# Optimization experiments

Measured on AMD Instinct MI355X. Metric: run time of the kernel, lower is better.

## Reference

```python
import jax, jax.numpy as jnp
import numpy as np

HID = 1024
NH = 16
HD = HID // NH  # 64


def _lin_params(key, fan_in, fan_out):
    k1, k2 = jax.random.split(key)
    lim = 1.0 / np.sqrt(fan_in)
    W = jax.random.uniform(k1, (fan_in, fan_out), jnp.float32, -lim, lim)
    b = jax.random.uniform(k2, (fan_out,), jnp.float32, -lim, lim)
    return W, b


def setup_inputs() -> dict:
    key = jax.random.key(0)
    ks = jax.random.split(key, 12)
    B, S = 4, 1024
    inp = {
        'query': jax.random.normal(ks[0], (B, S, HID), jnp.float32),
        'key': jax.random.normal(ks[1], (B, S, HID), jnp.float32),
        'value': jax.random.normal(ks[2], (B, S, HID), jnp.float32),
    }
    inp['Wq'], inp['bq'] = _lin_params(ks[3], HID, HID)
    inp['Wk'], inp['bk'] = _lin_params(ks[4], HID, HID)
    inp['Wv'], inp['bv'] = _lin_params(ks[5], HID, HID)
    inp['Wp'], inp['bp'] = _lin_params(ks[6], HID, HID)
    inp['Wup'], inp['bup'] = _lin_params(ks[7], HD, 1)
    inp['Wud'], inp['bud'] = _lin_params(ks[8], HD, 1)
    inp['Wus'], inp['bus'] = _lin_params(ks[9], HID, NH)
    inp['Wo'], inp['bo'] = _lin_params(ks[10], HID, HID)
    return inp


def _split_heads(x, B, S):
    # [B,S,HID] -> [B,NH,S,HD]
    return x.reshape(B, S, NH, HD).transpose(0, 2, 1, 3)


def reference(query, key, value, Wq, bq, Wk, bk, Wv, bv, Wp, bp,
              Wup, bup, Wud, bud, Wus, bus, Wo, bo):
    B, S, _ = query.shape
    len_q = S

    q = query @ Wq + bq   # [B,S,HID]
    k = key @ Wk + bk
    v = value @ Wv + bv

    # Gaussian-window positional bias (per head, per query position)
    p = _split_heads(q @ Wp + bp, B, S)              # [B,NH,S,HD]
    tp = jnp.tanh(p)
    p_i = tp @ Wup + bup                             # [B,NH,S,1]
    z_i = tp @ Wud + bud                             # [B,NH,S,1]
    cen_pos = len_q * jax.nn.sigmoid(p_i)            # [B,NH,S,1]
    win_size = len_q * jax.nn.sigmoid(z_i)           # [B,NH,S,1]
    pos = jnp.arange(len_q, dtype=q.dtype)[None, None, None, :]  # [1,1,1,S]
    bias = (pos - cen_pos) ** 2 / (0.5 * win_size ** 2)          # [B,NH,S,S]

    # per-head alpha gate from raw query
    alpha = jax.nn.sigmoid(query @ Wus + bus)        # [B,S,NH]
    alpha = alpha.reshape(B, S, NH, 1).transpose(0, 2, 1, 3)  # [B,NH,S,1]

    qh = _split_heads(q, B, S)
    kh = _split_heads(k, B, S)
    vh = _split_heads(v, B, S)

    scale = 1.0 / jnp.sqrt(jnp.asarray(HD, q.dtype))
    scores = jnp.einsum('bhqd,bhkd->bhqk', qh, kh) * scale
    scores = scores - alpha * bias                   # inject gated Gaussian bias
    attn = jax.nn.softmax(scores, axis=-1)           # [B,NH,S,S]

    out = jnp.einsum('bhqk,bhkd->bhqd', attn, vh)    # [B,NH,S,HD]
    x = out.transpose(0, 2, 1, 3).reshape(B, S, HID)
    x = x @ Wo + bo
    return x, attn
```

## Files before the change

### kernel.cpp

```cpp
#include <hip/hip_runtime.h>
#include <hip/hip_bf16.h>
#include <math.h>

#define S_LEN 1024
#define HIDN  1024
#define NHEAD 16
#define HDIM  64
#define BATCH 4
#define MTOT  (BATCH * S_LEN)

typedef __attribute__((ext_vector_type(8))) short          bf16v8;
typedef __attribute__((ext_vector_type(8))) unsigned short u16v8;
typedef __attribute__((ext_vector_type(4))) unsigned short u16v4;
typedef __attribute__((ext_vector_type(4))) float          f32v4;

__device__ __forceinline__ unsigned short f2bf_rne(float x) {
    unsigned int u = __float_as_uint(x);
    unsigned int r = (u + 0x7fffu + ((u >> 16) & 1u)) >> 16;
    return (unsigned short)r;
}
__device__ __forceinline__ float bf2f(unsigned short h) {
    return __uint_as_float(((unsigned int)h) << 16);
}
__device__ __forceinline__ void split2(float x, unsigned short& h, unsigned short& l) {
    h = f2bf_rne(x);
    l = f2bf_rne(x - bf2f(h));
}

__global__ __launch_bounds__(256) void split_a(
    const float* __restrict__ X, unsigned short* __restrict__ H,
    unsigned short* __restrict__ L)
{
    const int i = blockIdx.x * 256 + threadIdx.x;
    const float4 x0 = ((const float4*)X)[2 * i];
    const float4 x1 = ((const float4*)X)[2 * i + 1];
    float xs[8] = {x0.x, x0.y, x0.z, x0.w, x1.x, x1.y, x1.z, x1.w};
    u16v8 h, l;
#pragma unroll
    for (int j = 0; j < 8; ++j) {
        unsigned short hh, ll;
        split2(xs[j], hh, ll);
        h[j] = hh; l[j] = ll;
    }
    ((u16v8*)H)[i] = h;
    ((u16v8*)L)[i] = l;
}

__global__ __launch_bounds__(256) void split_w(
    const float* __restrict__ W, unsigned short* __restrict__ H,
    unsigned short* __restrict__ L)
{
    __shared__ float T[64][65];
    const int t  = threadIdx.x;
    const int k0 = blockIdx.y * 64;
    const int n0 = blockIdx.x * 64;

    const int r = t >> 4;
    const int c = (t & 15) * 4;
#pragma unroll
    for (int i = 0; i < 4; ++i) {
        const int rr = r + i * 16;
        const float4 v = *(const float4*)&W[(size_t)(k0 + rr) * 1024 + n0 + c];
        T[rr][c + 0] = v.x; T[rr][c + 1] = v.y;
        T[rr][c + 2] = v.z; T[rr][c + 3] = v.w;
    }
    __syncthreads();

    const int n  = t >> 2;
    const int ko = (t & 3) * 16;
    u16v8 h0, h1, l0, l1;
#pragma unroll
    for (int kk = 0; kk < 8; ++kk) {
        unsigned short hh, ll;
        split2(T[ko + kk][n], hh, ll);
        h0[kk] = hh; l0[kk] = ll;
    }
#pragma unroll
    for (int kk = 0; kk < 8; ++kk) {
        unsigned short hh, ll;
        split2(T[ko + 8 + kk][n], hh, ll);
        h1[kk] = hh; l1[kk] = ll;
    }
    unsigned short* Hp = &H[(size_t)(n0 + n) * 1024 + k0 + ko];
    unsigned short* Lp = &L[(size_t)(n0 + n) * 1024 + k0 + ko];
    *(u16v8*)(Hp)     = h0;
    *(u16v8*)(Hp + 8) = h1;
    *(u16v8*)(Lp)     = l0;
    *(u16v8*)(Lp + 8) = l1;
}

__global__ __launch_bounds__(512, 2) void gemm_bf16x3(
    const unsigned short* __restrict__ Ah, const unsigned short* __restrict__ Al,
    const unsigned short* __restrict__ Bh, const unsigned short* __restrict__ Bl,
    const float* __restrict__ bias, float* __restrict__ Cf,
    unsigned short* __restrict__ Ch, unsigned short* __restrict__ Cl, int vt)
{
    __shared__ short Ash[128][40];
    __shared__ short Asl[128][40];
    __shared__ short Bsh[64][40];
    __shared__ short Bsl[64][40];

    const int t    = threadIdx.x;
    const int bm   = blockIdx.y * 128;
    const int bn   = blockIdx.x * 64;
    const int lane = t & 63;
    const int wid  = t >> 6;
    const int wr   = wid >> 1;
    const int wc   = wid & 1;
    const int fr   = lane & 15;
    const int fq   = lane >> 4;
    const int ks   = fq * 8;

    f32v4 zero = {0.f, 0.f, 0.f, 0.f};
    f32v4 acc[2][2];
#pragma unroll
    for (int i = 0; i < 2; ++i)
#pragma unroll
        for (int j = 0; j < 2; ++j) acc[i][j] = zero;

    const int sra = t >> 2;
    const int sca = (t & 3) * 8;
    const int tb  = t & 255;
    const int srb = tb >> 2;
    const int scb = (tb & 3) * 8;
    const bool isBl = (t >= 256);
    const unsigned short* pAh = &Ah[(size_t)(bm + sra) * 1024 + sca];
    const unsigned short* pAl = &Al[(size_t)(bm + sra) * 1024 + sca];
    const unsigned short* pB  = isBl ? &Bl[(size_t)(bn + srb) * 1024 + scb]
                                     : &Bh[(size_t)(bn + srb) * 1024 + scb];

    u16v8 rah, ral, rb;
    auto LOAD = [&](int k0) {
        rah = *(const u16v8*)(pAh + k0);
        ral = *(const u16v8*)(pAl + k0);
        rb  = *(const u16v8*)(pB  + k0);
    };

    LOAD(0);
    for (int k0 = 0; k0 < 1024; k0 += 32) {
        __syncthreads();
        *(u16v8*)&Ash[sra][sca] = rah;
        *(u16v8*)&Asl[sra][sca] = ral;
        if (isBl) *(u16v8*)&Bsl[srb][scb] = rb;
        else      *(u16v8*)&Bsh[srb][scb] = rb;
        __syncthreads();

        if (k0 + 32 < 1024) LOAD(k0 + 32);

        bf16v8 fah[2], fal[2], fbh[2], fbl[2];
#pragma unroll
        for (int i = 0; i < 2; ++i) {
            fah[i] = *(const bf16v8*)&Ash[wr * 32 + i * 16 + fr][ks];
            fal[i] = *(const bf16v8*)&Asl[wr * 32 + i * 16 + fr][ks];
        }
#pragma unroll
        for (int j = 0; j < 2; ++j) {
            fbh[j] = *(const bf16v8*)&Bsh[wc * 32 + j * 16 + fr][ks];
            fbl[j] = *(const bf16v8*)&Bsl[wc * 32 + j * 16 + fr][ks];
        }
#pragma unroll
        for (int i = 0; i < 2; ++i)
#pragma unroll
            for (int j = 0; j < 2; ++j) {
                acc[i][j] = __builtin_amdgcn_mfma_f32_16x16x32_bf16(
                    fah[i], fbh[j], acc[i][j], 0, 0, 0);
                acc[i][j] = __builtin_amdgcn_mfma_f32_16x16x32_bf16(
                    fah[i], fbl[j], acc[i][j], 0, 0, 0);
                acc[i][j] = __builtin_amdgcn_mfma_f32_16x16x32_bf16(
                    fal[i], fbh[j], acc[i][j], 0, 0, 0);
            }
    }

#pragma unroll
    for (int j = 0; j < 2; ++j) {
        const int col = bn + wc * 32 + j * 16 + fr;
        const float bb = bias[col];
#pragma unroll
        for (int i = 0; i < 2; ++i) {
            const int row0 = bm + wr * 32 + i * 16 + fq * 4;
            const f32v4 cv = acc[i][j];
            if (vt) {
                u16v4 h4, l4;
#pragma unroll
                for (int r = 0; r < 4; ++r) {
                    unsigned short hh, ll;
                    split2(cv[r] + bb, hh, ll);
                    h4[r] = hh; l4[r] = ll;
                }
                const size_t base =
                    ((size_t)((row0 >> 10) * 16 + (col >> 6)) * 64 + (col & 63)) * 1024
                    + (row0 & 1023);
                *(u16v4*)&Ch[base] = h4;
                *(u16v4*)&Cl[base] = l4;
            } else {
#pragma unroll
                for (int r = 0; r < 4; ++r) {
                    const float v = cv[r] + bb;
                    const size_t idx = (size_t)(row0 + r) * 1024 + col;
                    if (Cf) Cf[idx] = v;
                    if (Ch) {
                        unsigned short hh, ll;
                        split2(v, hh, ll);
                        Ch[idx] = hh; Cl[idx] = ll;
                    }
                }
            }
        }
    }
}

__global__ __launch_bounds__(256) void alpha_kernel(
    const float* __restrict__ X, const float* __restrict__ Wus,
    const float* __restrict__ bus, float* __restrict__ alpha)
{
    __shared__ float Ws[1024 * 16];
    const int t = threadIdx.x;
#pragma unroll
    for (int i = 0; i < 16; ++i) {
        const int idx = t + i * 256;
        *reinterpret_cast<float4*>(&Ws[idx * 4]) =
            *reinterpret_cast<const float4*>(&Wus[idx * 4]);
    }
    __syncthreads();

    const int r = t >> 4, c = t & 15;
    const size_t row = (size_t)blockIdx.x * 16 + r;
    const float* x = &X[row * 1024];
    float acc = 0.f;
    for (int kk = 0; kk < 1024; kk += 4) {
        const float4 xv = *reinterpret_cast<const float4*>(&x[kk]);
        acc = fmaf(xv.x, Ws[(kk + 0) * 16 + c], acc);
        acc = fmaf(xv.y, Ws[(kk + 1) * 16 + c], acc);
        acc = fmaf(xv.z, Ws[(kk + 2) * 16 + c], acc);
        acc = fmaf(xv.w, Ws[(kk + 3) * 16 + c], acc);
    }
    acc += bus[c];
    alpha[row * 16 + c] = 1.f / (1.f + expf(-acc));
}

__global__ __launch_bounds__(256) void posparam_kernel(
    const float* __restrict__ p, const float* __restrict__ alpha,
    const float* __restrict__ Wup, const float* __restrict__ bup,
    const float* __restrict__ Wud, const float* __restrict__ bud,
    float* __restrict__ cen, float* __restrict__ c0)
{
    __shared__ float wu[64], wd[64];
    const int t = threadIdx.x;
    if (t < 64) { wu[t] = Wup[t]; wd[t] = Wud[t]; }
    __syncthreads();

    const int tid = blockIdx.x * 256 + t;
    const int b = tid >> 14;
    const int h = (tid >> 10) & 15;
    const int s = tid & 1023;

    const float* pr = &p[((size_t)(b * 1024 + s)) * 1024 + h * 64];
    float ap = 0.f, az = 0.f;
#pragma unroll
    for (int d = 0; d < 64; d += 4) {
        const float4 pv = *reinterpret_cast<const float4*>(&pr[d]);
        const float t0 = tanhf(pv.x), t1 = tanhf(pv.y);
        const float t2 = tanhf(pv.z), t3 = tanhf(pv.w);
        ap += t0 * wu[d] + t1 * wu[d + 1] + t2 * wu[d + 2] + t3 * wu[d + 3];
        az += t0 * wd[d] + t1 * wd[d + 1] + t2 * wd[d + 2] + t3 * wd[d + 3];
    }
    ap += bup[0];
    az += bud[0];
    const float cenv = 1024.f / (1.f + expf(-ap));
    const float win  = 1024.f / (1.f + expf(-az));
    const float al   = alpha[(size_t)(b * 1024 + s) * 16 + h];
    const int oi = (b * 16 + h) * 1024 + s;
    cen[oi] = cenv;
    c0[oi]  = al * 2.f / (win * win);
}

#define M0_SHIFT 8.0f
__global__ __launch_bounds__(512, 2) void attn_fused(
    const unsigned short* __restrict__ qh, const unsigned short* __restrict__ ql,
    const unsigned short* __restrict__ kh, const unsigned short* __restrict__ kl,
    const unsigned short* __restrict__ vTh, const unsigned short* __restrict__ vTl,
    const float* __restrict__ cen, const float* __restrict__ c0,
    float* __restrict__ attn,
    unsigned short* __restrict__ oh, unsigned short* __restrict__ ol)
{
    __shared__ unsigned short KH[64][64], KL[64][64];
    __shared__ unsigned short VH[64][64], VL[64][64];
    __shared__ unsigned short PH[128][64], PL[128][64];
    __shared__ float CEN[128], C0S[128];
    __shared__ float LSUM[2][128];
    __shared__ float RINV[128];

    const int bid   = blockIdx.x;
    const int z     = ((bid >> 6) << 3) | (bid & 7);
    const int itile = (bid >> 3) & 7;
    const int i0    = itile * 128;
    const int bq    = z >> 4;
    const int hd    = z & 15;

    const int t    = threadIdx.x;
    const int lane = t & 63;
    const int wid  = t >> 6;
    const int wrp  = wid >> 1;
    const int wc   = wid & 1;
    const int fr   = lane & 15, fq = lane >> 4;

    if (t < 128) {
        CEN[t] = cen[(size_t)z * 1024 + i0 + t];
        C0S[t] = c0[(size_t)z * 1024 + i0 + t];
    }

    bf16v8 qfh_[2][2], qfl_[2][2];
#pragma unroll
    for (int i = 0; i < 2; ++i)
#pragma unroll
        for (int kk = 0; kk < 2; ++kk) {
            const size_t qa = (size_t)(bq * 1024 + i0 + wrp * 32 + i * 16 + fr) * 1024
                              + hd * 64 + kk * 32 + fq * 8;
            qfh_[i][kk] = *(const bf16v8*)&qh[qa];
            qfl_[i][kk] = *(const bf16v8*)&ql[qa];
        }

    float lsum[2][4];
#pragma unroll
    for (int i = 0; i < 2; ++i)
#pragma unroll
        for (int r = 0; r < 4; ++r) lsum[i][r] = 0.f;

    const f32v4 zero = {0.f, 0.f, 0.f, 0.f};

    const int srow = t >> 3;
    const int sseg = t & 7;
    const int ssl  = (sseg ^ (srow & 7)) * 8;
    const unsigned short* vhb = vTh + (size_t)z * 64 * 1024;
    const unsigned short* vlb = vTl + (size_t)z * 64 * 1024;

    u16v8 rkh, rkl, rvh, rvl;
    auto LOADK = [&](int j0) {
        const size_t ga = (size_t)(bq * 1024 + j0 + srow) * 1024 + hd * 64 + sseg * 8;
        rkh = *(const u16v8*)&kh[ga];
        rkl = *(const u16v8*)&kl[ga];
    };
    auto LOADV = [&](int j0) {
        const size_t va = (size_t)srow * 1024 + j0 + sseg * 8;
        rvh = *(const u16v8*)&vhb[va];
        rvl = *(const u16v8*)&vlb[va];
    };

    LOADK(0);
    for (int jt = 0; jt < 16; ++jt) {
        const int j0 = jt * 64;
        __syncthreads();
        *(u16v8*)&KH[srow][ssl] = rkh;
        *(u16v8*)&KL[srow][ssl] = rkl;
        __syncthreads();
        if (jt < 15) LOADK(j0 + 64);

        f32v4 acc[2][2];
#pragma unroll
        for (int i = 0; i < 2; ++i)
#pragma unroll
            for (int j2 = 0; j2 < 2; ++j2) acc[i][j2] = zero;

#pragma unroll
        for (int kk = 0; kk < 2; ++kk) {
            bf16v8 fbh[2], fbl[2];
#pragma unroll
            for (int j2 = 0; j2 < 2; ++j2) {
                const int rb = wc * 32 + j2 * 16 + fr;
                const int sb = ((kk * 4 + fq) ^ (rb & 7)) * 8;
                fbh[j2] = *(const bf16v8*)&KH[rb][sb];
                fbl[j2] = *(const bf16v8*)&KL[rb][sb];
            }
#pragma unroll
            for (int i = 0; i < 2; ++i)
#pragma unroll
                for (int j2 = 0; j2 < 2; ++j2) {
                    acc[i][j2] = __builtin_amdgcn_mfma_f32_16x16x32_bf16(
                        qfh_[i][kk], fbh[j2], acc[i][j2], 0, 0, 0);
                    acc[i][j2] = __builtin_amdgcn_mfma_f32_16x16x32_bf16(
                        qfh_[i][kk], fbl[j2], acc[i][j2], 0, 0, 0);
                    acc[i][j2] = __builtin_amdgcn_mfma_f32_16x16x32_bf16(
                        qfl_[i][kk], fbh[j2], acc[i][j2], 0, 0, 0);
                }
        }

#pragma unroll
        for (int i = 0; i < 2; ++i)
#pragma unroll
            for (int r = 0; r < 4; ++r) {
                const int row = wrp * 32 + i * 16 + fq * 4 + r;
                const float cv = CEN[row], cc = C0S[row];
                float al = 0.f;
#pragma unroll
                for (int j2 = 0; j2 < 2; ++j2) {
                    const int col = wc * 32 + j2 * 16 + fr;
                    const float dd = (float)(j0 + col) - cv;
                    const float s  = acc[i][j2][r] * 0.125f - cc * dd * dd;
                    al += __expf(s - M0_SHIFT);
                }
                lsum[i][r] += al;
            }
    }

#pragma unroll
    for (int i = 0; i < 2; ++i)
#pragma unroll
        for (int r = 0; r < 4; ++r) {
            float v = lsum[i][r];
            v += __shfl_xor(v, 1);
            v += __shfl_xor(v, 2);
            v += __shfl_xor(v, 4);
            v += __shfl_xor(v, 8);
            if (fr == 0) LSUM[wc][wrp * 32 + i * 16 + fq * 4 + r] = v;
        }
    __syncthreads();
    if (t < 128) RINV[t] = 1.f / (LSUM[0][t] + LSUM[1][t]);

    f32v4 acco[2][2];
#pragma unroll
    for (int i = 0; i < 2; ++i)
#pragma unroll
        for (int j = 0; j < 2; ++j) acco[i][j] = zero;

    float* attnZ = attn + (size_t)z * 1024 * 1024;

    LOADK(0);
    LOADV(0);
    for (int jt = 0; jt < 16; ++jt) {
        const int j0 = jt * 64;
        __syncthreads();
        *(u16v8*)&KH[srow][ssl] = rkh;
        *(u16v8*)&KL[srow][ssl] = rkl;
        *(u16v8*)&VH[srow][ssl] = rvh;
        *(u16v8*)&VL[srow][ssl] = rvl;
        __syncthreads();
        if (jt < 15) { LOADK(j0 + 64); LOADV(j0 + 64); }

        f32v4 acc[2][2];
#pragma unroll
        for (int i = 0; i < 2; ++i)
#pragma unroll
            for (int j2 = 0; j2 < 2; ++j2) acc[i][j2] = zero;

#pragma unroll
        for (int kk = 0; kk < 2; ++kk) {
            bf16v8 fbh[2], fbl[2];
#pragma unroll
            for (int j2 = 0; j2 < 2; ++j2) {
                const int rb = wc * 32 + j2 * 16 + fr;
                const int sb = ((kk * 4 + fq) ^ (rb & 7)) * 8;
                fbh[j2] = *(const bf16v8*)&KH[rb][sb];
                fbl[j2] = *(const bf16v8*)&KL[rb][sb];
            }
#pragma unroll
            for (int i = 0; i < 2; ++i)
#pragma unroll
                for (int j2 = 0; j2 < 2; ++j2) {
                    acc[i][j2] = __builtin_amdgcn_mfma_f32_16x16x32_bf16(
                        qfh_[i][kk], fbh[j2], acc[i][j2], 0, 0, 0);
                    acc[i][j2] = __builtin_amdgcn_mfma_f32_16x16x32_bf16(
                        qfh_[i][kk], fbl[j2], acc[i][j2], 0, 0, 0);
                    acc[i][j2] = __builtin_amdgcn_mfma_f32_16x16x32_bf16(
                        qfl_[i][kk], fbh[j2], acc[i][j2], 0, 0, 0);
                }
        }

#pragma unroll
        for (int i = 0; i < 2; ++i)
#pragma unroll
            for (int r = 0; r < 4; ++r) {
                const int row = wrp * 32 + i * 16 + fq * 4 + r;
                const float cv = CEN[row], cc = C0S[row], ri = RINV[row];
#pragma unroll
                for (int j2 = 0; j2 < 2; ++j2) {
                    const int col = wc * 32 + j2 * 16 + fr;
                    const float dd = (float)(j0 + col) - cv;
                    const float s  = acc[i][j2][r] * 0.125f - cc * dd * dd;
                    const float p  = __expf(s - M0_SHIFT) * ri;
                    attnZ[(size_t)(i0 + row) * 1024 + j0 + col] = p;
                    unsigned short hv, lv;
                    split2(p, hv, lv);
                    const int slot = ((col >> 3) ^ (row & 7)) * 8 + (col & 7);
                    PH[row][slot] = hv;
                    PL[row][slot] = lv;
                }
            }
        __syncthreads();

#pragma unroll
        for (int kk = 0; kk < 2; ++kk) {
            bf16v8 pah[2], pal[2], fbh[2], fbl[2];
#pragma unroll
            for (int iq = 0; iq < 2; ++iq) {
                const int rp = wrp * 32 + iq * 16 + fr;
                const int sp = ((kk * 4 + fq) ^ (rp & 7)) * 8;
                pah[iq] = *(const bf16v8*)&PH[rp][sp];
                pal[iq] = *(const bf16v8*)&PL[rp][sp];
            }
#pragma unroll
            for (int jd = 0; jd < 2; ++jd) {
                const int rb = wc * 32 + jd * 16 + fr;
                const int sb = ((kk * 4 + fq) ^ (rb & 7)) * 8;
                fbh[jd] = *(const bf16v8*)&VH[rb][sb];
                fbl[jd] = *(const bf16v8*)&VL[rb][sb];
            }
#pragma unroll
            for (int iq = 0; iq < 2; ++iq)
#pragma unroll
                for (int jd = 0; jd < 2; ++jd) {
                    acco[iq][jd] = __builtin_amdgcn_mfma_f32_16x16x32_bf16(
                        pah[iq], fbh[jd], acco[iq][jd], 0, 0, 0);
                    acco[iq][jd] = __builtin_amdgcn_mfma_f32_16x16x32_bf16(
                        pah[iq], fbl[jd], acco[iq][jd], 0, 0, 0);
                    acco[iq][jd] = __builtin_amdgcn_mfma_f32_16x16x32_bf16(
                        pal[iq], fbh[jd], acco[iq][jd], 0, 0, 0);
                }
        }
    }

#pragma unroll
    for (int jd = 0; jd < 2; ++jd) {
        const int dcol = wc * 32 + jd * 16 + fr;
#pragma unroll
        for (int iq = 0; iq < 2; ++iq) {
            const int row0 = i0 + wrp * 32 + iq * 16 + fq * 4;
            const f32v4 cv = acco[iq][jd];
#pragma unroll
            for (int r = 0; r < 4; ++r) {
                unsigned short hv, lv;
                split2(cv[r], hv, lv);
                const size_t idx = (size_t)(bq * 1024 + row0 + r) * 1024 + hd * 64 + dcol;
                oh[idx] = hv;
                ol[idx] = lv;
            }
        }
    }
}

extern "C" void kernel_launch(void* const* d_in, const int* in_sizes, int n_in,
                              void* d_out, int out_size, void* d_ws, size_t ws_size,
                              hipStream_t stream)
{
    const float* query = (const float*)d_in[0];
    const float* key_  = (const float*)d_in[1];
    const float* value = (const float*)d_in[2];
    const float* Wq  = (const float*)d_in[3];
    const float* bq  = (const float*)d_in[4];
    const float* Wk  = (const float*)d_in[5];
    const float* bk  = (const float*)d_in[6];
    const float* Wv  = (const float*)d_in[7];
    const float* bv  = (const float*)d_in[8];
    const float* Wp  = (const float*)d_in[9];
    const float* bp  = (const float*)d_in[10];
    const float* Wup = (const float*)d_in[11];
    const float* bup = (const float*)d_in[12];
    const float* Wud = (const float*)d_in[13];
    const float* bud = (const float*)d_in[14];
    const float* Wus = (const float*)d_in[15];
    const float* bus = (const float*)d_in[16];
    const float* Wo  = (const float*)d_in[17];
    const float* bo  = (const float*)d_in[18];

    float* x_out = (float*)d_out;
    float* attn  = x_out + (size_t)MTOT * HIDN;

    char* wsb = (char*)d_ws;
    unsigned short* qh  = (unsigned short*)(wsb);
    unsigned short* ql  = (unsigned short*)(wsb + (8u  << 20));
    unsigned short* kh  = (unsigned short*)(wsb + (16u << 20));
    unsigned short* kl  = (unsigned short*)(wsb + (24u << 20));
    unsigned short* vTh = (unsigned short*)(wsb + (32u << 20));
    unsigned short* vTl = (unsigned short*)(wsb + (40u << 20));
    float* p_ws  = (float*)(wsb + (48u << 20));
    unsigned short* oh = (unsigned short*)(wsb + (48u << 20));
    unsigned short* ol = (unsigned short*)(wsb + (56u << 20));
    float* alpha_ws = (float*)(wsb + (64u << 20));
    float* cen_ws   = (float*)(wsb + (64u << 20) + (256u << 10));
    float* c0_ws    = (float*)(wsb + (64u << 20) + (512u << 10));
    unsigned short* ah = (unsigned short*)attn;
    unsigned short* al = ah + (size_t)MTOT * HIDN;
    unsigned short* wh = al + (size_t)MTOT * HIDN;
    unsigned short* wl = wh + (size_t)HIDN * HIDN;
    unsigned short* w2h = qh;
    unsigned short* w2l = ql;

    const dim3 blk(256);
    const dim3 blk512(512);
    const dim3 gsplit_a(MTOT * HIDN / 8 / 256);
    const dim3 gsplit_w(16, 16);
    const dim3 ggemm(HIDN / 64, MTOT / 128);

    split_w<<<gsplit_w, blk, 0, stream>>>(Wq, wh, wl);
    split_a<<<gsplit_a, blk, 0, stream>>>(query, ah, al);
    gemm_bf16x3<<<ggemm, blk512, 0, stream>>>(ah, al, wh, wl, bq, nullptr, qh, ql, 0);
    split_w<<<gsplit_w, blk, 0, stream>>>(Wk, wh, wl);
    split_a<<<gsplit_a, blk, 0, stream>>>(key_, ah, al);
    gemm_bf16x3<<<ggemm, blk512, 0, stream>>>(ah, al, wh, wl, bk, nullptr, kh, kl, 0);
    split_w<<<gsplit_w, blk, 0, stream>>>(Wv, wh, wl);
    split_a<<<gsplit_a, blk, 0, stream>>>(value, ah, al);
    gemm_bf16x3<<<ggemm, blk512, 0, stream>>>(ah, al, wh, wl, bv, nullptr, vTh, vTl, 1);
    split_w<<<gsplit_w, blk, 0, stream>>>(Wp, wh, wl);
    gemm_bf16x3<<<ggemm, blk512, 0, stream>>>(qh, ql, wh, wl, bp, p_ws, nullptr, nullptr, 0);
    alpha_kernel<<<dim3(MTOT / 16), blk, 0, stream>>>(query, Wus, bus, alpha_ws);
    posparam_kernel<<<dim3((BATCH * NHEAD * S_LEN) / 256), blk, 0, stream>>>(
        p_ws, alpha_ws, Wup, bup, Wud, bud, cen_ws, c0_ws);
    attn_fused<<<dim3(512), blk512, 0, stream>>>(
        qh, ql, kh, kl, vTh, vTl, cen_ws, c0_ws, attn, oh, ol);
    split_w<<<gsplit_w, blk, 0, stream>>>(Wo, w2h, w2l);
    gemm_bf16x3<<<ggemm, blk512, 0, stream>>>(oh, ol, w2h, w2l, bo, x_out,
                                              nullptr, nullptr, 0);
}
```

Before: 390.4 us.

## Fuse activation splitting into GEMM loads and posparam into projection epilogue

The fp32 activations for the Q/K/V projections are now split into bf16 hi/lo pairs inside the GEMM's global load stage, which removes the separate split_a kernels and their round-trip of the split arrays through memory. The four weight splits are batched into one launch over a z-grid. The Wp projection epilogue now applies tanh, the Wup/Wud dot products, sigmoid and the alpha gating directly, so the fp32 p tensor is never written out and the posparam kernel is dropped. The cost is extra conversion ALU work in each GEMM's load path, repeated for every column tile that reads the same activation rows, plus an extra shared-memory reduction and barrier in the fused epilogue.

```diff
diff --git a/kernel.cpp b/kernel.cpp
--- a/kernel.cpp
+++ b/kernel.cpp
@@ -27,33 +27,19 @@
     l = f2bf_rne(x - bf2f(h));
 }
 
-__global__ __launch_bounds__(256) void split_a(
-    const float* __restrict__ X, unsigned short* __restrict__ H,
-    unsigned short* __restrict__ L)
-{
-    const int i = blockIdx.x * 256 + threadIdx.x;
-    const float4 x0 = ((const float4*)X)[2 * i];
-    const float4 x1 = ((const float4*)X)[2 * i + 1];
-    float xs[8] = {x0.x, x0.y, x0.z, x0.w, x1.x, x1.y, x1.z, x1.w};
-    u16v8 h, l;
-#pragma unroll
-    for (int j = 0; j < 8; ++j) {
-        unsigned short hh, ll;
-        split2(xs[j], hh, ll);
-        h[j] = hh; l[j] = ll;
-    }
-    ((u16v8*)H)[i] = h;
-    ((u16v8*)L)[i] = l;
-}
-
-__global__ __launch_bounds__(256) void split_w(
-    const float* __restrict__ W, unsigned short* __restrict__ H,
-    unsigned short* __restrict__ L)
+__global__ __launch_bounds__(256) void split_w4(
+    const float* __restrict__ W0, const float* __restrict__ W1,
+    const float* __restrict__ W2, const float* __restrict__ W3,
+    unsigned short* __restrict__ Hbase, unsigned short* __restrict__ Lbase)
 {
     __shared__ float T[64][65];
     const int t  = threadIdx.x;
     const int k0 = blockIdx.y * 64;
     const int n0 = blockIdx.x * 64;
+    const int z  = blockIdx.z;
+    const float* W = (z == 0) ? W0 : (z == 1) ? W1 : (z == 2) ? W2 : W3;
+    unsigned short* H = Hbase + (size_t)z * 1024 * 1024;
+    unsigned short* L = Lbase + (size_t)z * 1024 * 1024;
 
     const int r = t >> 4;
     const int c = (t & 15) * 4;
@@ -89,16 +75,23 @@
     *(u16v8*)(Lp + 8) = l1;
 }
 
-__global__ __launch_bounds__(512, 2) void gemm_bf16x3(
+template<int AF32, int EPI>
+__global__ __launch_bounds__(512, 2) void gemm_t(
+    const float* __restrict__ Af,
     const unsigned short* __restrict__ Ah, const unsigned short* __restrict__ Al,
     const unsigned short* __restrict__ Bh, const unsigned short* __restrict__ Bl,
     const float* __restrict__ bias, float* __restrict__ Cf,
-    unsigned short* __restrict__ Ch, unsigned short* __restrict__ Cl, int vt)
+    unsigned short* __restrict__ Ch, unsigned short* __restrict__ Cl,
+    const float* __restrict__ Wup, const float* __restrict__ Wud,
+    const float* __restrict__ bup, const float* __restrict__ bud,
+    const float* __restrict__ alpha, float* __restrict__ cenp,
+    float* __restrict__ c0p)
 {
     __shared__ short Ash[128][40];
     __shared__ short Asl[128][40];
     __shared__ short Bsh[64][40];
     __shared__ short Bsl[64][40];
+    __shared__ float PSUP[2][128], PSUD[2][128];
 
     const int t    = threadIdx.x;
     const int bm   = blockIdx.y * 128;
@@ -124,16 +117,29 @@
     const int srb = tb >> 2;
     const int scb = (tb & 3) * 8;
     const bool isBl = (t >= 256);
-    const unsigned short* pAh = &Ah[(size_t)(bm + sra) * 1024 + sca];
-    const unsigned short* pAl = &Al[(size_t)(bm + sra) * 1024 + sca];
-    const unsigned short* pB  = isBl ? &Bl[(size_t)(bn + srb) * 1024 + scb]
-                                     : &Bh[(size_t)(bn + srb) * 1024 + scb];
+    const unsigned short* pB = isBl ? &Bl[(size_t)(bn + srb) * 1024 + scb]
+                                    : &Bh[(size_t)(bn + srb) * 1024 + scb];
+    const float* pAf = AF32 ? &Af[(size_t)(bm + sra) * 1024 + sca] : nullptr;
+    const unsigned short* pAh = AF32 ? nullptr : &Ah[(size_t)(bm + sra) * 1024 + sca];
+    const unsigned short* pAl = AF32 ? nullptr : &Al[(size_t)(bm + sra) * 1024 + sca];
 
     u16v8 rah, ral, rb;
     auto LOAD = [&](int k0) {
-        rah = *(const u16v8*)(pAh + k0);
-        ral = *(const u16v8*)(pAl + k0);
-        rb  = *(const u16v8*)(pB  + k0);
+        if (AF32) {
+            const float4 a0 = *(const float4*)(pAf + k0);
+            const float4 a1 = *(const float4*)(pAf + k0 + 4);
+            const float xs[8] = {a0.x, a0.y, a0.z, a0.w, a1.x, a1.y, a1.z, a1.w};
+#pragma unroll
+            for (int e = 0; e < 8; ++e) {
+                unsigned short hh, ll;
+                split2(xs[e], hh, ll);
+                rah[e] = hh; ral[e] = ll;
+            }
+        } else {
+            rah = *(const u16v8*)(pAh + k0);
+            ral = *(const u16v8*)(pAl + k0);
+        }
+        rb = *(const u16v8*)(pB + k0);
     };
 
     LOAD(0);
@@ -171,6 +177,63 @@
             }
     }
 
+    if (EPI == 3) {
+        float wupj[2], wudj[2];
+        float bb[2];
+#pragma unroll
+        for (int j = 0; j < 2; ++j) {
+            const int colL = wc * 32 + j * 16 + fr;
+            wupj[j] = Wup[colL];
+            wudj[j] = Wud[colL];
+            bb[j]   = bias[bn + colL];
+        }
+        float su[2][4], sd[2][4];
+#pragma unroll
+        for (int i = 0; i < 2; ++i)
+#pragma unroll
+            for (int r = 0; r < 4; ++r) { su[i][r] = 0.f; sd[i][r] = 0.f; }
+#pragma unroll
+        for (int j = 0; j < 2; ++j)
+#pragma unroll
+            for (int i = 0; i < 2; ++i)
+#pragma unroll
+                for (int r = 0; r < 4; ++r) {
+                    const float tv = tanhf(acc[i][j][r] + bb[j]);
+                    su[i][r] = fmaf(tv, wupj[j], su[i][r]);
+                    sd[i][r] = fmaf(tv, wudj[j], sd[i][r]);
+                }
+#pragma unroll
+        for (int i = 0; i < 2; ++i)
+#pragma unroll
+            for (int r = 0; r < 4; ++r) {
+                float a = su[i][r], d = sd[i][r];
+                a += __shfl_xor(a, 1); d += __shfl_xor(d, 1);
+                a += __shfl_xor(a, 2); d += __shfl_xor(d, 2);
+                a += __shfl_xor(a, 4); d += __shfl_xor(d, 4);
+                a += __shfl_xor(a, 8); d += __shfl_xor(d, 8);
+                if (fr == 0) {
+                    const int row = wr * 32 + i * 16 + fq * 4 + r;
+                    PSUP[wc][row] = a;
+                    PSUD[wc][row] = d;
+                }
+            }
+        __syncthreads();
+        if (t < 128) {
+            const float ap = PSUP[0][t] + PSUP[1][t] + bup[0];
+            const float az = PSUD[0][t] + PSUD[1][t] + bud[0];
+            const float cenv = 1024.f / (1.f + expf(-ap));
+            const float win  = 1024.f / (1.f + expf(-az));
+            const int grow = bm + t;
+            const int hd   = bn >> 6;
+            const int zz   = (grow >> 10) * 16 + hd;
+            const int s    = grow & 1023;
+            const float al = alpha[(size_t)grow * 16 + hd];
+            cenp[(size_t)zz * 1024 + s] = cenv;
+            c0p[(size_t)zz * 1024 + s]  = al * 2.f / (win * win);
+        }
+        return;
+    }
+
 #pragma unroll
     for (int j = 0; j < 2; ++j) {
         const int col = bn + wc * 32 + j * 16 + fr;
@@ -179,7 +242,7 @@
         for (int i = 0; i < 2; ++i) {
             const int row0 = bm + wr * 32 + i * 16 + fq * 4;
             const f32v4 cv = acc[i][j];
-            if (vt) {
+            if (EPI == 2) {
                 u16v4 h4, l4;
 #pragma unroll
                 for (int r = 0; r < 4; ++r) {
@@ -192,18 +255,18 @@
                     + (row0 & 1023);
                 *(u16v4*)&Ch[base] = h4;
                 *(u16v4*)&Cl[base] = l4;
+            } else if (EPI == 1) {
+#pragma unroll
+                for (int r = 0; r < 4; ++r) {
+                    unsigned short hh, ll;
+                    split2(cv[r] + bb, hh, ll);
+                    const size_t idx = (size_t)(row0 + r) * 1024 + col;
+                    Ch[idx] = hh; Cl[idx] = ll;
+                }
             } else {
 #pragma unroll
-                for (int r = 0; r < 4; ++r) {
-                    const float v = cv[r] + bb;
-                    const size_t idx = (size_t)(row0 + r) * 1024 + col;
-                    if (Cf) Cf[idx] = v;
-                    if (Ch) {
-                        unsigned short hh, ll;
-                        split2(v, hh, ll);
-                        Ch[idx] = hh; Cl[idx] = ll;
-                    }
-                }
+                for (int r = 0; r < 4; ++r)
+                    Cf[(size_t)(row0 + r) * 1024 + col] = cv[r] + bb;
             }
         }
     }
@@ -236,42 +299,6 @@
     }
     acc += bus[c];
     alpha[row * 16 + c] = 1.f / (1.f + expf(-acc));
-}
-
-__global__ __launch_bounds__(256) void posparam_kernel(
-    const float* __restrict__ p, const float* __restrict__ alpha,
-    const float* __restrict__ Wup, const float* __restrict__ bup,
-    const float* __restrict__ Wud, const float* __restrict__ bud,
-    float* __restrict__ cen, float* __restrict__ c0)
-{
-    __shared__ float wu[64], wd[64];
-    const int t = threadIdx.x;
-    if (t < 64) { wu[t] = Wup[t]; wd[t] = Wud[t]; }
-    __syncthreads();
-
-    const int tid = blockIdx.x * 256 + t;
-    const int b = tid >> 14;
-    const int h = (tid >> 10) & 15;
-    const int s = tid & 1023;
-
-    const float* pr = &p[((size_t)(b * 1024 + s)) * 1024 + h * 64];
-    float ap = 0.f, az = 0.f;
-#pragma unroll
-    for (int d = 0; d < 64; d += 4) {
-        const float4 pv = *reinterpret_cast<const float4*>(&pr[d]);
-        const float t0 = tanhf(pv.x), t1 = tanhf(pv.y);
-        const float t2 = tanhf(pv.z), t3 = tanhf(pv.w);
-        ap += t0 * wu[d] + t1 * wu[d + 1] + t2 * wu[d + 2] + t3 * wu[d + 3];
-        az += t0 * wd[d] + t1 * wd[d + 1] + t2 * wd[d + 2] + t3 * wd[d + 3];
-    }
-    ap += bup[0];
-    az += bud[0];
-    const float cenv = 1024.f / (1.f + expf(-ap));
-    const float win  = 1024.f / (1.f + expf(-az));
-    const float al   = alpha[(size_t)(b * 1024 + s) * 16 + h];
-    const int oi = (b * 16 + h) * 1024 + s;
-    cen[oi] = cenv;
-    c0[oi]  = al * 2.f / (win * win);
 }
 
 #define M0_SHIFT 8.0f
@@ -571,42 +598,41 @@
     unsigned short* kl  = (unsigned short*)(wsb + (24u << 20));
     unsigned short* vTh = (unsigned short*)(wsb + (32u << 20));
     unsigned short* vTl = (unsigned short*)(wsb + (40u << 20));
-    float* p_ws  = (float*)(wsb + (48u << 20));
-    unsigned short* oh = (unsigned short*)(wsb + (48u << 20));
-    unsigned short* ol = (unsigned short*)(wsb + (56u << 20));
+    unsigned short* oh  = (unsigned short*)(wsb + (48u << 20));
+    unsigned short* ol  = (unsigned short*)(wsb + (56u << 20));
     float* alpha_ws = (float*)(wsb + (64u << 20));
     float* cen_ws   = (float*)(wsb + (64u << 20) + (256u << 10));
     float* c0_ws    = (float*)(wsb + (64u << 20) + (512u << 10));
-    unsigned short* ah = (unsigned short*)attn;
-    unsigned short* al = ah + (size_t)MTOT * HIDN;
-    unsigned short* wh = al + (size_t)MTOT * HIDN;
-    unsigned short* wl = wh + (size_t)HIDN * HIDN;
+    unsigned short* wh = (unsigned short*)attn;
+    unsigned short* wl = wh + (size_t)4 * 1024 * 1024;
     unsigned short* w2h = qh;
     unsigned short* w2l = ql;
 
     const dim3 blk(256);
     const dim3 blk512(512);
-    const dim3 gsplit_a(MTOT * HIDN / 8 / 256);
-    const dim3 gsplit_w(16, 16);
     const dim3 ggemm(HIDN / 64, MTOT / 128);
-
-    split_w<<<gsplit_w, blk, 0, stream>>>(Wq, wh, wl);
-    split_a<<<gsplit_a, blk, 0, stream>>>(query, ah, al);
-    gemm_bf16x3<<<ggemm, blk512, 0, stream>>>(ah, al, wh, wl, bq, nullptr, qh, ql, 0);
-    split_w<<<gsplit_w, blk, 0, stream>>>(Wk, wh, wl);
-    split_a<<<gsplit_a, blk, 0, stream>>>(key_, ah, al);
-    gemm_bf16x3<<<ggemm, blk512, 0, stream>>>(ah, al, wh, wl, bk, nullptr, kh, kl, 0);
-    split_w<<<gsplit_w, blk, 0, stream>>>(Wv, wh, wl);
-    split_a<<<gsplit_a, blk, 0, stream>>>(value, ah, al);
-    gemm_bf16x3<<<ggemm, blk512, 0, stream>>>(ah, al, wh, wl, bv, nullptr, vTh, vTl, 1);
-    split_w<<<gsplit_w, blk, 0, stream>>>(Wp, wh, wl);
-    gemm_bf16x3<<<ggemm, blk512, 0, stream>>>(qh, ql, wh, wl, bp, p_ws, nullptr, nullptr, 0);
+    const size_t WSTEP = (size_t)1024 * 1024;
+
+    split_w4<<<dim3(16, 16, 4), blk, 0, stream>>>(Wq, Wk, Wv, Wp, wh, wl);
     alpha_kernel<<<dim3(MTOT / 16), blk, 0, stream>>>(query, Wus, bus, alpha_ws);
-    posparam_kernel<<<dim3((BATCH * NHEAD * S_LEN) / 256), blk, 0, stream>>>(
-        p_ws, alpha_ws, Wup, bup, Wud, bud, cen_ws, c0_ws);
+    gemm_t<1, 1><<<ggemm, blk512, 0, stream>>>(
+        query, nullptr, nullptr, wh, wl, bq, nullptr, qh, ql,
+        nullptr, nullptr, nullptr, nullptr, nullptr, nullptr, nullptr);
+    gemm_t<1, 1><<<ggemm, blk512, 0, stream>>>(
+        key_, nullptr, nullptr, wh + WSTEP, wl + WSTEP, bk, nullptr, kh, kl,
+        nullptr, nullptr, nullptr, nullptr, nullptr, nullptr, nullptr);
+    gemm_t<1, 2><<<ggemm, blk512, 0, stream>>>(
+        value, nullptr, nullptr, wh + 2 * WSTEP, wl + 2 * WSTEP, bv,
+        nullptr, vTh, vTl,
+        nullptr, nullptr, nullptr, nullptr, nullptr, nullptr, nullptr);
+    gemm_t<0, 3><<<ggemm, blk512, 0, stream>>>(
+        nullptr, qh, ql, wh + 3 * WSTEP, wl + 3 * WSTEP, bp, nullptr,
+        nullptr, nullptr,
+        Wup, Wud, bup, bud, alpha_ws, cen_ws, c0_ws);
     attn_fused<<<dim3(512), blk512, 0, stream>>>(
         qh, ql, kh, kl, vTh, vTl, cen_ws, c0_ws, attn, oh, ol);
-    split_w<<<gsplit_w, blk, 0, stream>>>(Wo, w2h, w2l);
-    gemm_bf16x3<<<ggemm, blk512, 0, stream>>>(oh, ol, w2h, w2l, bo, x_out,
-                                              nullptr, nullptr, 0);
-}
+    split_w4<<<dim3(16, 16, 1), blk, 0, stream>>>(Wo, Wo, Wo, Wo, w2h, w2l);
+    gemm_t<0, 0><<<ggemm, blk512, 0, stream>>>(
+        nullptr, oh, ol, w2h, w2l, bo, x_out, nullptr, nullptr,
+        nullptr, nullptr, nullptr, nullptr, nullptr, nullptr, nullptr);
+}
```

Result: faster. 379.9 us (-2.7%).
